# Kernel optimization log

Hardware: AMD Instinct MI355X
Metric: run time of the kernel (lower is better)

Reference implementation:

```python
import jax, jax.numpy as jnp
import numpy as np

RES = 256
XYZ_MIN, XYZ_MAX = -1.0, 1.0
STEPSIZE = 1.0
NEAR, FAR, BG = 0.2, 3.0, 1.0
ALPHA_INIT = 0.01
ACT_SHIFT = float(np.log(1.0 / (1.0 - ALPHA_INIT) - 1.0))
VOXEL = (XYZ_MAX - XYZ_MIN) / RES  # (prod(extent)/R^3)^(1/3) = 2/256
N_SAMPLES = int(np.linalg.norm(np.array([RES + 1] * 3, dtype=np.float64)) / STEPSIZE) + 1  # 446
N_RAYS = 4096
LATENT, NFEAT, RGB_LAT = 64, 32, 15
MULTIRES = 6


def _dense(key, din, dout):
    kw, kb = jax.random.split(key)
    return (jax.random.normal(kw, (din, dout), jnp.float32) / np.float32(np.sqrt(din)),
            jax.random.normal(kb, (dout,), jnp.float32) * 0.01)


def setup_inputs():
    ks = jax.random.split(jax.random.key(0), 16)
    rays_o = jax.random.normal(ks[0], (N_RAYS, 3), jnp.float32) * 1.5
    rays_d = jax.random.normal(ks[1], (N_RAYS, 3), jnp.float32)
    viewdirs = rays_d / jnp.linalg.norm(rays_d, axis=-1, keepdims=True)
    mW1, mb1 = _dense(ks[2], 4, 128)
    mW2, mb2 = _dense(ks[3], 128, 128)
    mW3, mb3 = _dense(ks[4], 128, NFEAT)
    pW1, pb1 = _dense(ks[5], LATENT, 64)
    pW2, pb2 = _dense(ks[6], 64, 64)
    pW3, pb3 = _dense(ks[7], 64, 1 + RGB_LAT)
    emb_dim = 3 + 3 * 2 * MULTIRES  # 39
    dW1, db1 = _dense(ks[8], RGB_LAT + emb_dim, 64)
    dW2, db2 = _dense(ks[9], 64, 64)
    dW3, db3 = _dense(ks[10], 64, 64)
    dW4, db4 = _dense(ks[11], 64, 3)
    return dict(
        rays_o=rays_o, rays_d=rays_d, viewdirs=viewdirs,
        mapping_grid=jax.random.normal(ks[12], (4, RES, RES, RES), jnp.float32) * 0.1,
        feature_vectors=jax.random.normal(ks[13], (NFEAT, LATENT), jnp.float32) * 0.1,
        mW1=mW1, mb1=mb1, mW2=mW2, mb2=mb2, mW3=mW3, mb3=mb3,
        pW1=pW1, pb1=pb1, pW2=pW2, pb2=pb2, pW3=pW3, pb3=pb3,
        dW1=dW1, db1=db1, dW2=dW2, db2=db2, dW3=dW3, db3=db3, dW4=dW4, db4=db4)


def _trilinear(grid, pts):
    # grid: [C,R,R,R]; pts: [...,3] world coords; matches F.grid_sample(align_corners=True)
    # after the flip(-1) in the original (x indexes dim0 of the volume).
    g = jnp.transpose(grid, (1, 2, 3, 0))  # [R,R,R,C]
    u = (pts - XYZ_MIN) / (XYZ_MAX - XYZ_MIN)
    idx = jnp.clip(u * (RES - 1), 0.0, RES - 1.0)
    i0 = jnp.clip(jnp.floor(idx).astype(jnp.int32), 0, RES - 2)
    f = idx - i0.astype(idx.dtype)
    x0, y0, z0 = i0[..., 0], i0[..., 1], i0[..., 2]
    x1, y1, z1 = x0 + 1, y0 + 1, z0 + 1
    fx, fy, fz = f[..., 0:1], f[..., 1:2], f[..., 2:3]
    c000, c001 = g[x0, y0, z0], g[x0, y0, z1]
    c010, c011 = g[x0, y1, z0], g[x0, y1, z1]
    c100, c101 = g[x1, y0, z0], g[x1, y0, z1]
    c110, c111 = g[x1, y1, z0], g[x1, y1, z1]
    c00 = c000 * (1 - fz) + c001 * fz
    c01 = c010 * (1 - fz) + c011 * fz
    c10 = c100 * (1 - fz) + c101 * fz
    c11 = c110 * (1 - fz) + c111 * fz
    c0 = c00 * (1 - fy) + c01 * fy
    c1 = c10 * (1 - fy) + c11 * fy
    return c0 * (1 - fx) + c1 * fx


def _mlp3(x, W1, b1, W2, b2, W3, b3):
    h = jax.nn.relu(x @ W1 + b1)
    h = jax.nn.relu(h @ W2 + b2)
    return h @ W3 + b3


def _dir_embed(v):
    # NeRF positional encoding: [v, sin(2^i v), cos(2^i v)] for i in [0, MULTIRES)
    freqs = 2.0 ** jnp.arange(MULTIRES, dtype=v.dtype)  # [L]
    ang = v[..., None, :] * freqs[:, None]              # [N,L,3]
    sc = jnp.concatenate([jnp.sin(ang), jnp.cos(ang)], axis=-1)  # [N,L,6]
    return jnp.concatenate([v, sc.reshape(v.shape[0], 2 * 3 * MULTIRES)], axis=-1)  # [N,39]


def reference(rays_o, rays_d, viewdirs, mapping_grid, feature_vectors,
              mW1, mb1, mW2, mb2, mW3, mb3,
              pW1, pb1, pW2, pb2, pW3, pb3,
              dW1, db1, dW2, db2, dW3, db3, dW4, db4):
    # --- ray sampling (is_train=False, no jitter) ---
    vec = jnp.where(rays_d == 0, 1e-6, rays_d)
    rate_a = (XYZ_MAX - rays_o) / vec
    rate_b = (XYZ_MIN - rays_o) / vec
    t_min = jnp.clip(jnp.minimum(rate_a, rate_b).max(-1), NEAR, FAR)
    t_max = jnp.clip(jnp.maximum(rate_a, rate_b).min(-1), NEAR, FAR)
    step = STEPSIZE * VOXEL * jnp.arange(N_SAMPLES, dtype=rays_o.dtype)  # [S]
    interpx = t_min[:, None] + step[None, :] / jnp.linalg.norm(rays_d, axis=-1, keepdims=True)
    ray_pts = rays_o[:, None, :] + rays_d[:, None, :] * interpx[..., None]  # [N,S,3]
    valid = ~((t_max <= t_min)[:, None]
              | jnp.any((ray_pts < XYZ_MIN) | (ray_pts > XYZ_MAX), axis=-1))  # [N,S]

    # --- latent extraction: grid sample -> attention over feature bank ---
    mp = _trilinear(mapping_grid, ray_pts)                                  # [N,S,4]
    attn = jax.nn.softmax(_mlp3(mp, mW1, mb1, mW2, mb2, mW3, mb3), axis=-1)  # [N,S,F]
    latent = attn @ feature_vectors                                          # [N,S,latent]

    # --- positional MLP -> density + rgb latent (masked entries zeroed as in torch) ---
    pos = _mlp3(latent, pW1, pb1, pW2, pb2, pW3, pb3)  # [N,S,1+rgb_lat]
    alpha = jnp.where(valid,
                      1.0 - jnp.exp(-jax.nn.softplus(pos[..., 0] + ACT_SHIFT) * STEPSIZE),
                      0.0)
    rgb_latent = jnp.where(valid[..., None], pos[..., 1:], 0.0)

    # --- alpha compositing weights ---
    alphainv_cum = jnp.concatenate(
        [jnp.ones_like(alpha[..., :1]),
         jnp.cumprod(jnp.clip(1.0 - alpha, 1e-10, None), axis=-1)], axis=-1)  # [N,S+1]
    weights = alpha * alphainv_cum[..., :-1]

    # --- directional MLP -> rgb ---
    emb = _dir_embed(viewdirs)                                               # [N,39]
    emb = jnp.broadcast_to(emb[:, None, :], (alpha.shape[0], alpha.shape[1], emb.shape[-1]))
    rgb_feat = jnp.concatenate([rgb_latent, emb], axis=-1)                   # [N,S,54]
    h = jax.nn.relu(rgb_feat @ dW1 + db1)
    h = jax.nn.relu(h @ dW2 + db2)
    h = jax.nn.relu(h @ dW3 + db3)
    raw_rgb = h @ dW4 + db4
    rgb = jnp.where(valid[..., None], jax.nn.sigmoid(raw_rgb[..., :3]), 0.0)

    rgb_marched = jnp.einsum('ns,nsc->nc', weights, rgb) + alphainv_cum[..., -1:] * BG
    return rgb_marched
```

## Files before the change

kernel.cpp:

```cpp
#include <hip/hip_runtime.h>
#include <math.h>

#define ACT_SHIFT -4.5951198501345889f
#define SB 128
#define NSLOTMAX (4096*446)

typedef _Float16 f16;
typedef f16 f16x8 __attribute__((ext_vector_type(8)));
typedef f16 f16x4 __attribute__((ext_vector_type(4)));
typedef float f32x4 __attribute__((ext_vector_type(4)));
typedef float f32x16 __attribute__((ext_vector_type(16)));

#define OFF_CNT  0
#define OFF_RAYI 256
#define OFF_RAYF (OFF_RAYI + 4096*16)
#define OFF_EMBW (OFF_RAYF + 4096*8)
#define OFF_WTS  (OFF_EMBW + 4096*64*4)
#define OFF_BIAS (OFF_WTS + 92160)
#define OFF_SLOT (OFF_BIAS + 8192)
#define OFF_WS4H (OFF_SLOT + NSLOTMAX*4)

#define W_MW1 0
#define W_MW2 2048
#define W_MW3 18432
#define W_FV  22528
#define W_P1  24576
#define W_P2  28672
#define W_P3  32768
#define W_D1  34816
#define W_D2  35840
#define W_D3  39936
#define W_D4  44032
#define W_TOT 46080

static __device__ __forceinline__ unsigned short f2h(float x) {
  f16 h = (f16)x; return *(unsigned short*)&h;
}
static __device__ __forceinline__ float h2f(unsigned short u) {
  return (float)(*(f16*)&u);
}

static __device__ __forceinline__ void bar_lds() {
  asm volatile("s_waitcnt lgkmcnt(0)" ::: "memory");
  __builtin_amdgcn_s_barrier();
}

static __device__ __forceinline__ void sample_point(
    float ox, float oy, float oz, float dx, float dy, float dz,
    float tmin, float nrm, int s, float& px, float& py, float& pz) {
  float ix = tmin + (0.0078125f * (float)s) / nrm;
  px = ox + dx * ix; py = oy + dy * ix; pz = oz + dz * ix;
}
static __device__ __forceinline__ int in_box(float px, float py, float pz) {
  return !(px < -1.f || px > 1.f || py < -1.f || py > 1.f ||
           pz < -1.f || pz > 1.f);
}

static __device__ __forceinline__ bool ray_setup(
    const float* rays_o, const float* rays_d, int r,
    float& ox, float& oy, float& oz, float& dx, float& dy, float& dz,
    float& tmin, float& nrm) {
  ox = rays_o[r*3+0]; oy = rays_o[r*3+1]; oz = rays_o[r*3+2];
  dx = rays_d[r*3+0]; dy = rays_d[r*3+1]; dz = rays_d[r*3+2];
  const float vx = (dx == 0.0f) ? 1e-6f : dx;
  const float vy = (dy == 0.0f) ? 1e-6f : dy;
  const float vz = (dz == 0.0f) ? 1e-6f : dz;
  const float rax = ( 1.0f - ox) / vx, rbx = (-1.0f - ox) / vx;
  const float ray_ = ( 1.0f - oy) / vy, rby = (-1.0f - oy) / vy;
  const float raz = ( 1.0f - oz) / vz, rbz = (-1.0f - oz) / vz;
  tmin = fmaxf(fmaxf(fminf(rax,rbx), fminf(ray_,rby)), fminf(raz,rbz));
  tmin = fminf(fmaxf(tmin, 0.2f), 3.0f);
  float tmax = fminf(fminf(fmaxf(rax,rbx), fmaxf(ray_,rby)), fmaxf(raz,rbz));
  tmax = fminf(fmaxf(tmax, 0.2f), 3.0f);
  nrm = sqrtf(dx*dx + dy*dy + dz*dz);
  return tmax <= tmin;
}

// ... 44 lines not shown
      const float* __restrict__ mb1, const float* __restrict__ mb2,
      const float* __restrict__ mb3, const float* __restrict__ pb1,
      const float* __restrict__ pb2, const float* __restrict__ pb3,
      const float* __restrict__ db1, const float* __restrict__ db2,
      const float* __restrict__ db3, const float* __restrict__ db4,
      f16* __restrict__ wts, float* __restrict__ bias,
      float* __restrict__ embW) {
  const int b = blockIdx.x, t = threadIdx.x;
  if (b < 1024) {
    int idx = b * 256 + t;
    int ray = idx >> 6, o = idx & 63;
    float v0 = viewdirs[ray*3+0], v1 = viewdirs[ray*3+1], v2 = viewdirs[ray*3+2];
    float acc = db1[o];
    acc = fmaf(v0, dW1[15*64+o], acc);
    acc = fmaf(v1, dW1[16*64+o], acc);
    acc = fmaf(v2, dW1[17*64+o], acc);
#pragma unroll
    for (int fr = 0; fr < 6; ++fr) {
      float f = (float)(1 << fr);
      int rb = 18 + fr*6;
      acc = fmaf(sinf(v0*f), dW1[(rb+0)*64+o], acc);
      acc = fmaf(sinf(v1*f), dW1[(rb+1)*64+o], acc);
      acc = fmaf(sinf(v2*f), dW1[(rb+2)*64+o], acc);
      acc = fmaf(cosf(v0*f), dW1[(rb+3)*64+o], acc);
      acc = fmaf(cosf(v1*f), dW1[(rb+4)*64+o], acc);
      acc = fmaf(cosf(v2*f), dW1[(rb+5)*64+o], acc);
    }
    embW[idx] = acc;
  } else if (b < 1280) {
    int ray = (b - 1024) * 16 + (t >> 4);
    int4 ri = rayi[ray];
    for (int i = t & 15; i < ri.z; i += 16)
      slot_map[ri.x + i] = (ray << 9) | (ri.y + i);
  } else if (b < 1460) {
    int i = (b - 1280) * 256 + t;
    if (i >= W_TOT) return;
    float v = 0.f; int l, o, k;
    if (i < W_MW2)      { l=i;        o=l>>4; k=l&15;  if (k<4)  v = mW1[k*128+o]; }
    else if (i < W_MW3) { l=i-W_MW2;  o=l>>7; k=l&127; v = mW2[k*128+o]; }
    else if (i < W_FV)  { l=i-W_MW3;  o=l>>7; k=l&127; v = mW3[k*32+o]; }
    else if (i < W_P1)  { l=i-W_FV;   o=l>>5; k=l&31;  v = fv[k*64+o]; }
    else if (i < W_P2)  { l=i-W_P1;   o=l>>6; k=l&63;  v = pW1[k*64+o]; }
    else if (i < W_P3)  { l=i-W_P2;   o=l>>6; k=l&63;  v = pW2[k*64+o]; }
    else if (i < W_D1)  { l=i-W_P3;   o=l>>6; k=l&63;  if (o<16) v = pW3[k*16+o]; }
    else if (i < W_D2)  { l=i-W_D1;   o=l>>4; k=l&15;  if (k>=1) v = dW1[(k-1)*64+o]; }
    else if (i < W_D3)  { l=i-W_D2;   o=l>>6; k=l&63;  v = dW2[k*64+o]; }
    else if (i < W_D4)  { l=i-W_D3;   o=l>>6; k=l&63;  v = dW3[k*64+o]; }
    else                { l=i-W_D4;   o=l>>6; k=l&63;  if (o<3)  v = dW4[k*3+o]; }
    wts[i] = (f16)v;
  } else {
    int i = (b - 1460) * 256 + t;
    if (i >= 1408) return;
    int L = i >> 7, o = i & 127;
    float v = 0.f;
    if      (L == 0)            v = mb1[o];
    else if (L == 1)            v = mb2[o];
    else if (L == 2 && o < 32)  v = mb3[o];
    else if (L == 4 && o < 64)  v = pb1[o];
    else if (L == 5 && o < 64)  v = pb2[o];
    else if (L == 6 && o < 16)  v = pb3[o];
    else if (L == 8 && o < 64)  v = db2[o];
    else if (L == 9 && o < 64)  v = db3[o];
    else if (L == 10 && o < 3)  v = db4[o];
    bias[i] = v;
  }
}

template<int KS>
static __device__ __forceinline__ void load_b(const f16* Xb, int st, int lane,
                                              f16x8* B) {
  const int r = st*32 + (lane & 31);
  const int base = r*256 + ((lane >> 5) * 16);
#pragma unroll
  for (int ks = 0; ks < KS; ++ks) {
    int off = (base + ks*32) ^ ((r & 15) << 4);
    B[ks] = *(const f16x8*)((const char*)Xb + off);
  }
}

template<int KS>
static __device__ __forceinline__ void load_a(const f16* __restrict__ wbase,
                                              int dt, int lane, f16x8* A) {
  const f16* wp = wbase + (size_t)(dt*32 + (lane & 31)) * (KS*16) + (lane >> 5) * 8;
#pragma unroll
  for (int ks = 0; ks < KS; ++ks) A[ks] = *(const f16x8*)(wp + ks*16);
}

template<int KS>
static __device__ __forceinline__ f32x16 mm(const f16x8* A, const f16x8* B) {
  f32x16 acc;
#pragma unroll
  for (int i = 0; i < 16; ++i) acc[i] = 0.f;
#pragma unroll
  for (int ks = 0; ks < KS; ++ks)
    acc = __builtin_amdgcn_mfma_f32_32x32x16_f16(A[ks], B[ks], acc, 0, 0, 0);
  return acc;
}

template<bool RELU, int NQ>
static __device__ __forceinline__ void store_c(f16* Yb, int st, int dtb, int lane,
                                               const f32x16& acc,
                                               const float* __restrict__ bp) {
  const int r = st*32 + (lane & 31);
  const int gp = (lane >> 5) * 4;
#pragma unroll
  for (int q = 0; q < NQ; ++q) {
    const int db = dtb + q*8 + gp;
    f32x4 b4 = *(const f32x4*)(bp + db);
    float v0 = acc[4*q+0]+b4[0], v1 = acc[4*q+1]+b4[1];
    float v2 = acc[4*q+2]+b4[2], v3 = acc[4*q+3]+b4[3];
    if (RELU) {
      v0 = fmaxf(v0,0.f); v1 = fmaxf(v1,0.f);
      v2 = fmaxf(v2,0.f); v3 = fmaxf(v3,0.f);
    }
    f16x4 o = {(f16)v0,(f16)v1,(f16)v2,(f16)v3};
    int off = (r*256 + db*2) ^ ((r & 15) << 4);
    *(f16x4*)((char*)Yb + off) = o;
  }
}

struct Pf {
  float v[8];
  float fx, fy, fz;
  int pk;
};

static __device__ __forceinline__ void pf_issue(
    int slot, int total, int c,
    const int* __restrict__ slot_map, const float2* __restrict__ rayf,
    const float* __restrict__ rays_o, const float* __restrict__ rays_d,
    const float* __restrict__ grid, Pf& P) {
  if (slot >= total) {
    P.pk = -2; P.fx = P.fy = P.fz = 0.f;
#pragma unroll
    for (int i = 0; i < 8; ++i) P.v[i] = 0.f;
    return;
  }
  int mi = slot_map[slot];
  int ray = mi >> 9, s = mi & 511;
  float2 tf = rayf[ray];
  float ox = rays_o[ray*3+0], oy = rays_o[ray*3+1], oz = rays_o[ray*3+2];
  float dx = rays_d[ray*3+0], dy = rays_d[ray*3+1], dz = rays_d[ray*3+2];
  float px, py, pz;
  sample_point(ox,oy,oz,dx,dy,dz, tf.x, tf.y, s, px,py,pz);
  P.pk = ray*2 + in_box(px,py,pz);
  float ixf = fminf(fmaxf((px + 1.f) * 0.5f * 255.f, 0.f), 255.f);
  float iyf = fminf(fmaxf((py + 1.f) * 0.5f * 255.f, 0.f), 255.f);
  float izf = fminf(fmaxf((pz + 1.f) * 0.5f * 255.f, 0.f), 255.f);
  int x0 = min((int)ixf, 254), y0 = min((int)iyf, 254), z0 = min((int)izf, 254);
  P.fx = ixf - (float)x0; P.fy = iyf - (float)y0; P.fz = izf - (float)z0;
  const float* gc = grid + (size_t)c * 16777216u;
  int bx0 = x0 << 16, bx1 = bx0 + 65536;
  int by0 = y0 << 8,  by1 = by0 + 256;
  P.v[0] = gc[bx0+by0+z0]; P.v[1] = gc[bx0+by0+z0+1];
  P.v[2] = gc[bx0+by1+z0]; P.v[3] = gc[bx0+by1+z0+1];
  P.v[4] = gc[bx1+by0+z0]; P.v[5] = gc[bx1+by0+z0+1];
  P.v[6] = gc[bx1+by1+z0]; P.v[7] = gc[bx1+by1+z0+1];
}

extern "C" __global__ void __launch_bounds__(512)
k_mlp(const float* __restrict__ rays_o, const float* __restrict__ rays_d,
      const float* __restrict__ grid, const int* __restrict__ slot_map,
      const float2* __restrict__ rayf, const float* __restrict__ embW,
      const f16* __restrict__ wts, const float* __restrict__ bias,
      int* __restrict__ cnt, unsigned short* __restrict__ ws4h) {
  const int total = cnt[0];
  const int nch = (total + 127) >> 7;
  int* qh = cnt + 1;
  const int tid = threadIdx.x;
  const int wv = tid >> 6, lane = tid & 63;
  const int sl = tid >> 2, ch = tid & 3;
  const int dthi = wv >> 2;
  const int stw = wv & 3;

  __shared__ __align__(16) f16 X[SB*128];
  __shared__ __align__(16) f16 Y[SB*128];
  __shared__ int sinfo[SB];
  __shared__ int q_next;

  f16x8 aMW1a[1], aMW1b[1], aFV[2], aP1[4], aP2[4], aD1[1], aD2[4], aD3[4];
  load_a<1>(wts+W_MW1, dthi,   lane, aMW1a);
  load_a<1>(wts+W_MW1, dthi+2, lane, aMW1b);
  load_a<2>(wts+W_FV,  dthi,   lane, aFV);
  load_a<4>(wts+W_P1,  dthi,   lane, aP1);
  load_a<4>(wts+W_P2,  dthi,   lane, aP2);
  load_a<1>(wts+W_D1,  dthi,   lane, aD1);
  load_a<4>(wts+W_D2,  dthi,   lane, aD2);
  load_a<4>(wts+W_D3,  dthi,   lane, aD3);
  f16x8 aP3[4], aD4[4];
  if (wv < 4) {
    load_a<4>(wts+W_P3, 0, lane, aP3);
    load_a<4>(wts+W_D4, 0, lane, aD4);
  }

  if (tid == 0) q_next = atomicAdd(qh, 1);
  __syncthreads();
  int cur = q_next;

  Pf P;
  pf_issue((cur < nch) ? cur*128 + sl : total, total, ch,
           slot_map, rayf, rays_o, rays_d, grid, P);

  while (cur < nch) {
    const int blockbase = cur << 7;
    if (tid == 0) q_next = atomicAdd(qh, 1);

    {
      float c00 = P.v[0]*(1.f-P.fz) + P.v[1]*P.fz;
      float c01 = P.v[2]*(1.f-P.fz) + P.v[3]*P.fz;
      float c10 = P.v[4]*(1.f-P.fz) + P.v[5]*P.fz;
      float c11 = P.v[6]*(1.f-P.fz) + P.v[7]*P.fz;
      float c0v = c00*(1.f-P.fy) + c01*P.fy;
      float c1v = c10*(1.f-P.fy) + c11*P.fy;
      float mv  = c0v*(1.f-P.fx) + c1v*P.fx;
      if (ch == 0) sinfo[sl] = P.pk;
      int off = (sl*256 + ch*2) ^ ((sl & 15) << 4);
      *(f16*)((char*)X + off) = (f16)mv;
      if (ch < 3) {
        int zo = (sl*256 + 8 + ch*8) ^ ((sl & 15) << 4);
        *(unsigned long long*)((char*)X + zo) = 0ull;
      }
    }
    bar_lds();
    const int nxt = q_next;
    pf_issue((nxt < nch) ? nxt*128 + sl : total, total, ch,
             slot_map, rayf, rays_o, rays_d, grid, P);

    float alpha_reg = 0.f; int pk_reg = -2;

    { f16x8 B[1]; load_b<1>(X, stw, lane, B);
      f32x16 a0 = mm<1>(aMW1a, B);
      store_c<true,4>(Y, stw, dthi*32, lane, a0, bias + 0*128);
      f32x16 a1 = mm<1>(aMW1b, B);
      store_c<true,4>(Y, stw, (dthi+2)*32, lane, a1, bias + 0*128);
    } bar_lds();

    { f16x8 B[8]; load_b<8>(Y, stw, lane, B);
      f16x8 A8[8];
      load_a<8>(wts+W_MW2, dthi, lane, A8);
      f32x16 a0 = mm<8>(A8, B);
      store_c<true,4>(X, stw, dthi*32, lane, a0, bias + 1*128);
      load_a<8>(wts+W_MW2, dthi+2, lane, A8);
      f32x16 a1 = mm<8>(A8, B);
      store_c<true,4>(X, stw, (dthi+2)*32, lane, a1, bias + 1*128);
    } bar_lds();

    if (wv < 4) {
      f16x8 B[8]; load_b<8>(X, wv, lane, B);
      f16x8 A8[8]; load_a<8>(wts+W_MW3, 0, lane, A8);
      f32x16 acc = mm<8>(A8, B);
      const int gp = (lane >> 5) * 4;
      float v[16];
#pragma unroll
      for (int q = 0; q < 4; ++q) {
        f32x4 b4 = *(const f32x4*)(bias + 2*128 + q*8 + gp);
#pragma unroll
        for (int i = 0; i < 4; ++i) v[4*q+i] = acc[4*q+i] + b4[i];
      }
      float mx = v[0];
#pragma unroll
      for (int i = 1; i < 16; ++i) mx = fmaxf(mx, v[i]);
      mx = fmaxf(mx, __shfl_xor(mx, 32));
      float s = 0.f;
#pragma unroll
      for (int i = 0; i < 16; ++i) { v[i] = expf(v[i] - mx); s += v[i]; }
      s += __shfl_xor(s, 32);
      float inv = 1.f / s;
      const int r = wv*32 + (lane & 31);
#pragma unroll
      for (int q = 0; q < 4; ++q) {
        const int db = q*8 + gp;
        f16x4 o = {(f16)(v[4*q+0]*inv), (f16)(v[4*q+1]*inv),
                   (f16)(v[4*q+2]*inv), (f16)(v[4*q+3]*inv)};
        int off = (r*256 + db*2) ^ ((r & 15) << 4);
        *(f16x4*)((char*)Y + off) = o;
      }
    }
    bar_lds();

    { f16x8 B[2]; load_b<2>(Y, stw, lane, B);
      f32x16 a0 = mm<2>(aFV, B);
      store_c<false,4>(X, stw, dthi*32, lane, a0, bias + 3*128);
    } bar_lds();

    { f16x8 B[4]; load_b<4>(X, stw, lane, B);
      f32x16 a0 = mm<4>(aP1, B);
      store_c<true,4>(Y, stw, dthi*32, lane, a0, bias + 4*128);
    } bar_lds();

    { f16x8 B[4]; load_b<4>(Y, stw, lane, B);
      f32x16 a0 = mm<4>(aP2, B);
      store_c<true,4>(X, stw, dthi*32, lane, a0, bias + 5*128);
    } bar_lds();

    if (wv < 4) {
      f16x8 B[4]; load_b<4>(X, wv, lane, B);
      f32x16 acc = mm<4>(aP3, B);
      pk_reg = sinfo[wv*32 + (lane & 31)];
      if (lane < 32) {
        alpha_reg = 0.f;
        if (pk_reg >= 0 && (pk_reg & 1)) {
          float x = acc[0] + bias[6*128 + 0] + ACT_SHIFT;
          float sp = fmaxf(x, 0.f) + log1pf(expf(-fabsf(x)));
          alpha_reg = 1.f - expf(-sp);
        }
      }
      store_c<false,2>(Y, wv, 0, lane, acc, bias + 6*128);
    }
    bar_lds();

    { f16x8 B[1]; load_b<1>(Y, stw, lane, B);
      f32x16 acc = mm<1>(aD1, B);
      int pkc = sinfo[stw*32 + (lane & 31)];
      int ry = (pkc < 0) ? 0 : (pkc >> 1);
      store_c<true,4>(X, stw, dthi*32, lane, acc, embW + (size_t)ry*64);
    } bar_lds();

    { f16x8 B[4]; load_b<4>(X, stw, lane, B);
      f32x16 a0 = mm<4>(aD2, B);
      store_c<true,4>(Y, stw, dthi*32, lane, a0, bias + 8*128);
    } bar_lds();

    { f16x8 B[4]; load_b<4>(Y, stw, lane, B);
      f32x16 a0 = mm<4>(aD3, B);
      store_c<true,4>(X, stw, dthi*32, lane, a0, bias + 9*128);
    } bar_lds();

    if (wv < 4) {
      f16x8 B[4]; load_b<4>(X, wv, lane, B);
      f32x16 acc = mm<4>(aD4, B);
      if (lane < 32 && pk_reg >= 0) {
        const float* bp = bias + 10*128;
        bool val = (pk_reg & 1) != 0;
        ushort4 u;
        u.x = f2h(alpha_reg);
        u.y = f2h(val ? 1.f/(1.f+expf(-(acc[0]+bp[0]))) : 0.f);
        u.z = f2h(val ? 1.f/(1.f+expf(-(acc[1]+bp[1]))) : 0.f);
        u.w = f2h(val ? 1.f/(1.f+expf(-(acc[2]+bp[2]))) : 0.f);
        *(ushort4*)(ws4h + (size_t)(blockbase + wv*32 + (lane & 31))*4) = u;
      }
    }
    bar_lds();
    cur = nxt;
  }
}

extern "C" __global__ void __launch_bounds__(256)
k_scan(const ushort4* __restrict__ ws4h, const int4* __restrict__ rayi,
       float* __restrict__ out) {
  const int wid = (blockIdx.x * 256 + threadIdx.x) >> 6;
  const int ln  = threadIdx.x & 63;
  if (wid >= 4096) return;
  int4 ri = rayi[wid];
  int base = ri.x, n_s = ri.z;

  float T = 1.0f, ar = 0.f, ag = 0.f, ab = 0.f;
  int nc = (n_s + 63) >> 6;
  for (int cck = 0; cck < nc; ++cck) {
    int j = cck*64 + ln;
    float a = 0.f, rr = 0.f, gg = 0.f, bb = 0.f;
    if (j < n_s) {
      ushort4 u = ws4h[(size_t)base + j];
      a = h2f(u.x); rr = h2f(u.y); gg = h2f(u.z); bb = h2f(u.w);
    }
    float p = fmaxf(1.0f - a, 1e-10f);
#pragma unroll
    for (int off = 1; off < 64; off <<= 1) {
      float o = __shfl_up(p, off);
      if (ln >= off) p *= o;
    }
    float pe = __shfl_up(p, 1);
    if (ln == 0) pe = 1.0f;
    float wgt = a * T * pe;
    ar = fmaf(wgt, rr, ar);
    ag = fmaf(wgt, gg, ag);
    ab = fmaf(wgt, bb, ab);
// ... 14 lines not shown

extern "C" void kernel_launch(void* const* d_in, const int* in_sizes, int n_in,
                              void* d_out, int out_size, void* d_ws, size_t ws_size,
                              hipStream_t stream) {
  const float* rays_o   = (const float*)d_in[0];
  const float* rays_d   = (const float*)d_in[1];
  const float* viewdirs = (const float*)d_in[2];
  const float* grid     = (const float*)d_in[3];
  const float* fv       = (const float*)d_in[4];
  const float* mW1 = (const float*)d_in[5];  const float* mb1 = (const float*)d_in[6];
  const float* mW2 = (const float*)d_in[7];  const float* mb2 = (const float*)d_in[8];
  const float* mW3 = (const float*)d_in[9];  const float* mb3 = (const float*)d_in[10];
  const float* pW1 = (const float*)d_in[11]; const float* pb1 = (const float*)d_in[12];
  const float* pW2 = (const float*)d_in[13]; const float* pb2 = (const float*)d_in[14];
  const float* pW3 = (const float*)d_in[15]; const float* pb3 = (const float*)d_in[16];
  const float* dW1 = (const float*)d_in[17]; const float* db1 = (const float*)d_in[18];
  const float* dW2 = (const float*)d_in[19]; const float* db2 = (const float*)d_in[20];
  const float* dW3 = (const float*)d_in[21]; const float* db3 = (const float*)d_in[22];
  const float* dW4 = (const float*)d_in[23]; const float* db4 = (const float*)d_in[24];
  float* out = (float*)d_out;

  char* ws = (char*)d_ws;
  int*     cnt      = (int*)(ws + OFF_CNT);
  int4*    rayi     = (int4*)(ws + OFF_RAYI);
  float2*  rayf     = (float2*)(ws + OFF_RAYF);
  float*   embW     = (float*)(ws + OFF_EMBW);
  f16*     wts      = (f16*)(ws + OFF_WTS);
  float*   bias     = (float*)(ws + OFF_BIAS);
  int*     slot_map = (int*)(ws + OFF_SLOT);
  unsigned short* ws4h = (unsigned short*)(ws + OFF_WS4H);

  hipMemsetAsync(cnt, 0, 8, stream);
  k_setup<<<16, 256, 0, stream>>>(rays_o, rays_d, cnt, rayi, rayf);
  k_aux<<<1466, 256, 0, stream>>>(viewdirs, rayi, slot_map,
                                  mW1, mW2, mW3, fv, pW1, pW2, pW3,
                                  dW1, dW2, dW3, dW4,
                                  mb1, mb2, mb3, pb1, pb2, pb3,
                                  db1, db2, db3, db4, wts, bias, embW);
  k_mlp<<<256, 512, 0, stream>>>(rays_o, rays_d, grid, slot_map, rayf,
                                 embW, wts, bias, cnt, ws4h);
  k_scan<<<1024, 256, 0, stream>>>((const ushort4*)ws4h, rayi, out);
}
```

Before: 103.2 us.

## Restructure MLP kernel into single-wave blocks processing 32-sample groups

Replaces the persistent 512-thread workgroup, which used an atomic work queue and barriers between layers over 128-sample tiles, with 64-thread single-wave blocks. Each block handles 32 samples with a grid-stride loop, so all layers run inside one wave with no LDS barriers. Weights are now read from global/L1 per layer instead of being held in registers, and each lane gathers two grid channels instead of one. The first-layer K dimension is padded to 32 so the weight layouts fit the new loops. This trades away inter-wave weight register reuse and the dynamic load balancing of the queue for more occupancy and less synchronisation.

```diff
diff --git a/kernel.cpp b/kernel.cpp
--- a/kernel.cpp
+++ b/kernel.cpp
@@ -2,12 +2,13 @@
 #include <math.h>
 
 #define ACT_SHIFT -4.5951198501345889f
-#define SB 128
 #define NSLOTMAX (4096*446)
+#define MLP_BLOCKS 2560
 
 typedef _Float16 f16;
 typedef f16 f16x8 __attribute__((ext_vector_type(8)));
 typedef f16 f16x4 __attribute__((ext_vector_type(4)));
+typedef f16 f16x2 __attribute__((ext_vector_type(2)));
 typedef float f32x4 __attribute__((ext_vector_type(4)));
 typedef float f32x16 __attribute__((ext_vector_type(16)));
 
@@ -16,33 +17,28 @@
 #define OFF_RAYF (OFF_RAYI + 4096*16)
 #define OFF_EMBW (OFF_RAYF + 4096*8)
 #define OFF_WTS  (OFF_EMBW + 4096*64*4)
-#define OFF_BIAS (OFF_WTS + 92160)
+#define OFF_BIAS (OFF_WTS + 98304)
 #define OFF_SLOT (OFF_BIAS + 8192)
 #define OFF_WS4H (OFF_SLOT + NSLOTMAX*4)
 
 #define W_MW1 0
-#define W_MW2 2048
-#define W_MW3 18432
-#define W_FV  22528
-#define W_P1  24576
-#define W_P2  28672
-#define W_P3  32768
-#define W_D1  34816
-#define W_D2  35840
-#define W_D3  39936
-#define W_D4  44032
-#define W_TOT 46080
+#define W_MW2 4096
+#define W_MW3 20480
+#define W_FV  24576
+#define W_P1  26624
+#define W_P2  30720
+#define W_P3  34816
+#define W_D1  36864
+#define W_D2  38912
+#define W_D3  43008
+#define W_D4  47104
+#define W_TOT 49152
 
 static __device__ __forceinline__ unsigned short f2h(float x) {
   f16 h = (f16)x; return *(unsigned short*)&h;
 }
 static __device__ __forceinline__ float h2f(unsigned short u) {
   return (float)(*(f16*)&u);
-}
-
-static __device__ __forceinline__ void bar_lds() {
-  asm volatile("s_waitcnt lgkmcnt(0)" ::: "memory");
-  __builtin_amdgcn_s_barrier();
 }
 
 static __device__ __forceinline__ void sample_point(
@@ -153,24 +149,24 @@
     int4 ri = rayi[ray];
     for (int i = t & 15; i < ri.z; i += 16)
       slot_map[ri.x + i] = (ray << 9) | (ri.y + i);
-  } else if (b < 1460) {
+  } else if (b < 1472) {
     int i = (b - 1280) * 256 + t;
     if (i >= W_TOT) return;
     float v = 0.f; int l, o, k;
-    if (i < W_MW2)      { l=i;        o=l>>4; k=l&15;  if (k<4)  v = mW1[k*128+o]; }
+    if (i < W_MW2)      { l=i;        o=l>>5; k=l&31;  if (k<4) v = mW1[k*128+o]; }
     else if (i < W_MW3) { l=i-W_MW2;  o=l>>7; k=l&127; v = mW2[k*128+o]; }
     else if (i < W_FV)  { l=i-W_MW3;  o=l>>7; k=l&127; v = mW3[k*32+o]; }
     else if (i < W_P1)  { l=i-W_FV;   o=l>>5; k=l&31;  v = fv[k*64+o]; }
     else if (i < W_P2)  { l=i-W_P1;   o=l>>6; k=l&63;  v = pW1[k*64+o]; }
     else if (i < W_P3)  { l=i-W_P2;   o=l>>6; k=l&63;  v = pW2[k*64+o]; }
     else if (i < W_D1)  { l=i-W_P3;   o=l>>6; k=l&63;  if (o<16) v = pW3[k*16+o]; }
-    else if (i < W_D2)  { l=i-W_D1;   o=l>>4; k=l&15;  if (k>=1) v = dW1[(k-1)*64+o]; }
+    else if (i < W_D2)  { l=i-W_D1;   o=l>>5; k=l&31;  if (k>=1 && k<16) v = dW1[(k-1)*64+o]; }
     else if (i < W_D3)  { l=i-W_D2;   o=l>>6; k=l&63;  v = dW2[k*64+o]; }
     else if (i < W_D4)  { l=i-W_D3;   o=l>>6; k=l&63;  v = dW3[k*64+o]; }
     else                { l=i-W_D4;   o=l>>6; k=l&63;  if (o<3)  v = dW4[k*3+o]; }
     wts[i] = (f16)v;
   } else {
-    int i = (b - 1460) * 256 + t;
+    int i = (b - 1472) * 256 + t;
     if (i >= 1408) return;
     int L = i >> 7, o = i & 127;
     float v = 0.f;
@@ -187,74 +183,192 @@
   }
 }
 
+static __device__ __forceinline__ f32x16 mfma16(f16x8 a, f16x8 b, f32x16 c) {
+  return __builtin_amdgcn_mfma_f32_32x32x16_f16(a, b, c, 0, 0, 0);
+}
+
 template<int KS>
-static __device__ __forceinline__ void load_b(const f16* Xb, int st, int lane,
-                                              f16x8* B) {
-  const int r = st*32 + (lane & 31);
-  const int base = r*256 + ((lane >> 5) * 16);
-#pragma unroll
-  for (int ks = 0; ks < KS; ++ks) {
-    int off = (base + ks*32) ^ ((r & 15) << 4);
-    B[ks] = *(const f16x8*)((const char*)Xb + off);
-  }
-}
-
-template<int KS>
-static __device__ __forceinline__ void load_a(const f16* __restrict__ wbase,
-                                              int dt, int lane, f16x8* A) {
-  const f16* wp = wbase + (size_t)(dt*32 + (lane & 31)) * (KS*16) + (lane >> 5) * 8;
-#pragma unroll
-  for (int ks = 0; ks < KS; ++ks) A[ks] = *(const f16x8*)(wp + ks*16);
-}
-
-template<int KS>
-static __device__ __forceinline__ f32x16 mm(const f16x8* A, const f16x8* B) {
+static __device__ __forceinline__ void load_B(const f16* Xi, int lane, f16x8* B) {
+  const int c = lane & 31;
+  const int sw = (c & 15) << 4;
+  const int rbase = c*256 + (lane >> 5) * 16;
+#pragma unroll
+  for (int ks = 0; ks < KS; ++ks)
+    B[ks] = *(const f16x8*)((const char*)Xi + ((rbase + ks*32) ^ sw));
+}
+
+template<int KS, int MT, bool RELU>
+static __device__ __forceinline__ void layerN(
+    const f16* __restrict__ W, const float* __restrict__ bp,
+    const f16* Xi, f16* Yo, int lane) {
+  const int c = lane & 31, g = lane >> 5;
+  const int sw = (c & 15) << 4;
+  f16x8 B[KS];
+  load_B<KS>(Xi, lane, B);
+#pragma unroll
+  for (int dt = 0; dt < MT; ++dt) {
+    f32x16 acc;
+#pragma unroll
+    for (int i = 0; i < 16; ++i) acc[i] = 0.f;
+    const f16* wp = W + (size_t)(dt*32 + c)*(KS*16) + g*8;
+#pragma unroll
+    for (int ks = 0; ks < KS; ++ks)
+      acc = mfma16(*(const f16x8*)(wp + ks*16), B[ks], acc);
+#pragma unroll
+    for (int q = 0; q < 4; ++q) {
+      const int db = dt*32 + q*8 + g*4;
+      f32x4 b4 = *(const f32x4*)(bp + db);
+      float v0 = acc[4*q+0]+b4[0], v1 = acc[4*q+1]+b4[1];
+      float v2 = acc[4*q+2]+b4[2], v3 = acc[4*q+3]+b4[3];
+      if (RELU) {
+        v0 = fmaxf(v0,0.f); v1 = fmaxf(v1,0.f);
+        v2 = fmaxf(v2,0.f); v3 = fmaxf(v3,0.f);
+      }
+      f16x4 o = {(f16)v0,(f16)v1,(f16)v2,(f16)v3};
+      *(f16x4*)((char*)Yo + ((c*256 + db*2) ^ sw)) = o;
+    }
+  }
+}
+
+static __device__ __forceinline__ void layer_emb(
+    const f16* __restrict__ W, const float* __restrict__ embR,
+    const f16* Xi, f16* Yo, int lane) {
+  const int c = lane & 31, g = lane >> 5;
+  const int sw = (c & 15) << 4;
+  f16x8 B[2];
+  load_B<2>(Xi, lane, B);
+#pragma unroll
+  for (int dt = 0; dt < 2; ++dt) {
+    f32x16 acc;
+#pragma unroll
+    for (int i = 0; i < 16; ++i) acc[i] = 0.f;
+    const f16* wp = W + (size_t)(dt*32 + c)*32 + g*8;
+#pragma unroll
+    for (int ks = 0; ks < 2; ++ks)
+      acc = mfma16(*(const f16x8*)(wp + ks*16), B[ks], acc);
+#pragma unroll
+    for (int q = 0; q < 4; ++q) {
+      const int db = dt*32 + q*8 + g*4;
+      f32x4 b4 = *(const f32x4*)(embR + db);
+      float v0 = fmaxf(acc[4*q+0]+b4[0], 0.f), v1 = fmaxf(acc[4*q+1]+b4[1], 0.f);
+      float v2 = fmaxf(acc[4*q+2]+b4[2], 0.f), v3 = fmaxf(acc[4*q+3]+b4[3], 0.f);
+      f16x4 o = {(f16)v0,(f16)v1,(f16)v2,(f16)v3};
+      *(f16x4*)((char*)Yo + ((c*256 + db*2) ^ sw)) = o;
+    }
+  }
+}
+
+static __device__ __forceinline__ void layer_mw3(
+    const f16* __restrict__ W, const float* __restrict__ bp,
+    const f16* Xi, f16* Yo, int lane) {
+  const int c = lane & 31, g = lane >> 5;
+  const int sw = (c & 15) << 4;
+  f16x8 B[8];
+  load_B<8>(Xi, lane, B);
   f32x16 acc;
 #pragma unroll
   for (int i = 0; i < 16; ++i) acc[i] = 0.f;
-#pragma unroll
-  for (int ks = 0; ks < KS; ++ks)
-    acc = __builtin_amdgcn_mfma_f32_32x32x16_f16(A[ks], B[ks], acc, 0, 0, 0);
-  return acc;
-}
-
-template<bool RELU, int NQ>
-static __device__ __forceinline__ void store_c(f16* Yb, int st, int dtb, int lane,
-                                               const f32x16& acc,
-                                               const float* __restrict__ bp) {
-  const int r = st*32 + (lane & 31);
-  const int gp = (lane >> 5) * 4;
-#pragma unroll
-  for (int q = 0; q < NQ; ++q) {
-    const int db = dtb + q*8 + gp;
+  const f16* wp = W + (size_t)c*128 + g*8;
+#pragma unroll
+  for (int ks = 0; ks < 8; ++ks)
+    acc = mfma16(*(const f16x8*)(wp + ks*16), B[ks], acc);
+  float v[16];
+#pragma unroll
+  for (int q = 0; q < 4; ++q) {
+    f32x4 b4 = *(const f32x4*)(bp + q*8 + g*4);
+#pragma unroll
+    for (int i = 0; i < 4; ++i) v[4*q+i] = acc[4*q+i] + b4[i];
+  }
+  float mx = v[0];
+#pragma unroll
+  for (int i = 1; i < 16; ++i) mx = fmaxf(mx, v[i]);
+  mx = fmaxf(mx, __shfl_xor(mx, 32));
+  float s = 0.f;
+#pragma unroll
+  for (int i = 0; i < 16; ++i) { v[i] = expf(v[i] - mx); s += v[i]; }
+  s += __shfl_xor(s, 32);
+  float inv = 1.f / s;
+#pragma unroll
+  for (int q = 0; q < 4; ++q) {
+    const int db = q*8 + g*4;
+    f16x4 o = {(f16)(v[4*q+0]*inv), (f16)(v[4*q+1]*inv),
+               (f16)(v[4*q+2]*inv), (f16)(v[4*q+3]*inv)};
+    *(f16x4*)((char*)Yo + ((c*256 + db*2) ^ sw)) = o;
+  }
+}
+
+static __device__ __forceinline__ void layer_p3(
+    const f16* __restrict__ W, const float* __restrict__ bp,
+    const f16* Xi, f16* Yo, int lane, int pks, float& alpha) {
+  const int c = lane & 31, g = lane >> 5;
+  const int sw = (c & 15) << 4;
+  f16x8 B[4];
+  load_B<4>(Xi, lane, B);
+  f32x16 acc;
+#pragma unroll
+  for (int i = 0; i < 16; ++i) acc[i] = 0.f;
+  const f16* wp = W + (size_t)c*64 + g*8;
+#pragma unroll
+  for (int ks = 0; ks < 4; ++ks)
+    acc = mfma16(*(const f16x8*)(wp + ks*16), B[ks], acc);
+  if (g == 0) {
+    alpha = 0.f;
+    if (pks >= 0 && (pks & 1)) {
+      float x = acc[0] + bp[0] + ACT_SHIFT;
+      float sp = fmaxf(x, 0.f) + log1pf(expf(-fabsf(x)));
+      alpha = 1.f - expf(-sp);
+    }
+  }
+#pragma unroll
+  for (int q = 0; q < 4; ++q) {
+    const int db = q*8 + g*4;
     f32x4 b4 = *(const f32x4*)(bp + db);
-    float v0 = acc[4*q+0]+b4[0], v1 = acc[4*q+1]+b4[1];
-    float v2 = acc[4*q+2]+b4[2], v3 = acc[4*q+3]+b4[3];
-    if (RELU) {
-      v0 = fmaxf(v0,0.f); v1 = fmaxf(v1,0.f);
-      v2 = fmaxf(v2,0.f); v3 = fmaxf(v3,0.f);
-    }
-    f16x4 o = {(f16)v0,(f16)v1,(f16)v2,(f16)v3};
-    int off = (r*256 + db*2) ^ ((r & 15) << 4);
-    *(f16x4*)((char*)Yb + off) = o;
+    f16x4 o = {(f16)(acc[4*q+0]+b4[0]), (f16)(acc[4*q+1]+b4[1]),
+               (f16)(acc[4*q+2]+b4[2]), (f16)(acc[4*q+3]+b4[3])};
+    *(f16x4*)((char*)Yo + ((c*256 + db*2) ^ sw)) = o;
+  }
+}
+
+static __device__ __forceinline__ void layer_d4(
+    const f16* __restrict__ W, const float* __restrict__ bp,
+    const f16* Xi, int lane, int pks, float alpha,
+    unsigned short* __restrict__ ws4h, int base) {
+  const int c = lane & 31, g = lane >> 5;
+  f16x8 B[4];
+  load_B<4>(Xi, lane, B);
+  f32x16 acc;
+#pragma unroll
+  for (int i = 0; i < 16; ++i) acc[i] = 0.f;
+  const f16* wp = W + (size_t)c*64 + g*8;
+#pragma unroll
+  for (int ks = 0; ks < 4; ++ks)
+    acc = mfma16(*(const f16x8*)(wp + ks*16), B[ks], acc);
+  if (g == 0 && pks >= 0) {
+    bool val = (pks & 1) != 0;
+    ushort4 u;
+    u.x = f2h(alpha);
+    u.y = f2h(val ? 1.f/(1.f+expf(-(acc[0]+bp[0]))) : 0.f);
+    u.z = f2h(val ? 1.f/(1.f+expf(-(acc[1]+bp[1]))) : 0.f);
+    u.w = f2h(val ? 1.f/(1.f+expf(-(acc[2]+bp[2]))) : 0.f);
+    *(ushort4*)(ws4h + (size_t)(base + c)*4) = u;
   }
 }
 
 struct Pf {
-  float v[8];
+  float v[16];
   float fx, fy, fz;
   int pk;
 };
 
 static __device__ __forceinline__ void pf_issue(
-    int slot, int total, int c,
+    int slot, int total, int cpair,
     const int* __restrict__ slot_map, const float2* __restrict__ rayf,
     const float* __restrict__ rays_o, const float* __restrict__ rays_d,
     const float* __restrict__ grid, Pf& P) {
   if (slot >= total) {
     P.pk = -2; P.fx = P.fy = P.fz = 0.f;
 #pragma unroll
-    for (int i = 0; i < 8; ++i) P.v[i] = 0.f;
+    for (int i = 0; i < 16; ++i) P.v[i] = 0.f;
     return;
   }
   int mi = slot_map[slot];
@@ -270,199 +384,89 @@
   float izf = fminf(fmaxf((pz + 1.f) * 0.5f * 255.f, 0.f), 255.f);
   int x0 = min((int)ixf, 254), y0 = min((int)iyf, 254), z0 = min((int)izf, 254);
   P.fx = ixf - (float)x0; P.fy = iyf - (float)y0; P.fz = izf - (float)z0;
-  const float* gc = grid + (size_t)c * 16777216u;
   int bx0 = x0 << 16, bx1 = bx0 + 65536;
   int by0 = y0 << 8,  by1 = by0 + 256;
-  P.v[0] = gc[bx0+by0+z0]; P.v[1] = gc[bx0+by0+z0+1];
-  P.v[2] = gc[bx0+by1+z0]; P.v[3] = gc[bx0+by1+z0+1];
-  P.v[4] = gc[bx1+by0+z0]; P.v[5] = gc[bx1+by0+z0+1];
-  P.v[6] = gc[bx1+by1+z0]; P.v[7] = gc[bx1+by1+z0+1];
-}
-
-extern "C" __global__ void __launch_bounds__(512)
+#pragma unroll
+  for (int q = 0; q < 2; ++q) {
+    const float* gc = grid + (size_t)(cpair*2 + q) * 16777216u;
+    P.v[q*8+0] = gc[bx0+by0+z0]; P.v[q*8+1] = gc[bx0+by0+z0+1];
+    P.v[q*8+2] = gc[bx0+by1+z0]; P.v[q*8+3] = gc[bx0+by1+z0+1];
+    P.v[q*8+4] = gc[bx1+by0+z0]; P.v[q*8+5] = gc[bx1+by0+z0+1];
+    P.v[q*8+6] = gc[bx1+by1+z0]; P.v[q*8+7] = gc[bx1+by1+z0+1];
+  }
+}
+
+extern "C" __global__ void __launch_bounds__(64)
 k_mlp(const float* __restrict__ rays_o, const float* __restrict__ rays_d,
       const float* __restrict__ grid, const int* __restrict__ slot_map,
       const float2* __restrict__ rayf, const float* __restrict__ embW,
       const f16* __restrict__ wts, const float* __restrict__ bias,
-      int* __restrict__ cnt, unsigned short* __restrict__ ws4h) {
+      const int* __restrict__ cnt, unsigned short* __restrict__ ws4h) {
   const int total = cnt[0];
-  const int nch = (total + 127) >> 7;
-  int* qh = cnt + 1;
-  const int tid = threadIdx.x;
-  const int wv = tid >> 6, lane = tid & 63;
-  const int sl = tid >> 2, ch = tid & 3;
-  const int dthi = wv >> 2;
-  const int stw = wv & 3;
-
-  __shared__ __align__(16) f16 X[SB*128];
-  __shared__ __align__(16) f16 Y[SB*128];
-  __shared__ int sinfo[SB];
-  __shared__ int q_next;
-
-  f16x8 aMW1a[1], aMW1b[1], aFV[2], aP1[4], aP2[4], aD1[1], aD2[4], aD3[4];
-  load_a<1>(wts+W_MW1, dthi,   lane, aMW1a);
-  load_a<1>(wts+W_MW1, dthi+2, lane, aMW1b);
-  load_a<2>(wts+W_FV,  dthi,   lane, aFV);
-  load_a<4>(wts+W_P1,  dthi,   lane, aP1);
-  load_a<4>(wts+W_P2,  dthi,   lane, aP2);
-  load_a<1>(wts+W_D1,  dthi,   lane, aD1);
-  load_a<4>(wts+W_D2,  dthi,   lane, aD2);
-  load_a<4>(wts+W_D3,  dthi,   lane, aD3);
-  f16x8 aP3[4], aD4[4];
-  if (wv < 4) {
-    load_a<4>(wts+W_P3, 0, lane, aP3);
-    load_a<4>(wts+W_D4, 0, lane, aD4);
-  }
-
-  if (tid == 0) q_next = atomicAdd(qh, 1);
-  __syncthreads();
-  int cur = q_next;
-
+  const int ngrp = (total + 31) >> 5;
+  const int lane = threadIdx.x;
+  const int sl = lane >> 1, cp = lane & 1;
+  const int c = lane & 31;
+
+  __shared__ __align__(16) f16 X[32*128];
+  __shared__ __align__(16) f16 Y[32*128];
+
+  int grp = blockIdx.x;
   Pf P;
-  pf_issue((cur < nch) ? cur*128 + sl : total, total, ch,
+  pf_issue((grp < ngrp) ? grp*32 + sl : total, total, cp,
            slot_map, rayf, rays_o, rays_d, grid, P);
 
-  while (cur < nch) {
-    const int blockbase = cur << 7;
-    if (tid == 0) q_next = atomicAdd(qh, 1);
-
+  for (; grp < ngrp; grp += gridDim.x) {
     {
-      float c00 = P.v[0]*(1.f-P.fz) + P.v[1]*P.fz;
-      float c01 = P.v[2]*(1.f-P.fz) + P.v[3]*P.fz;
-      float c10 = P.v[4]*(1.f-P.fz) + P.v[5]*P.fz;
-      float c11 = P.v[6]*(1.f-P.fz) + P.v[7]*P.fz;
-      float c0v = c00*(1.f-P.fy) + c01*P.fy;
-      float c1v = c10*(1.f-P.fy) + c11*P.fy;
-      float mv  = c0v*(1.f-P.fx) + c1v*P.fx;
-      if (ch == 0) sinfo[sl] = P.pk;
-      int off = (sl*256 + ch*2) ^ ((sl & 15) << 4);
-      *(f16*)((char*)X + off) = (f16)mv;
-      if (ch < 3) {
-        int zo = (sl*256 + 8 + ch*8) ^ ((sl & 15) << 4);
-        *(unsigned long long*)((char*)X + zo) = 0ull;
+      const int swr = (sl & 15) << 4;
+      float m[2];
+#pragma unroll
+      for (int q = 0; q < 2; ++q) {
+        const float* vv = P.v + q*8;
+        float c00 = vv[0]*(1.f-P.fz) + vv[1]*P.fz;
+        float c01 = vv[2]*(1.f-P.fz) + vv[3]*P.fz;
+        float c10 = vv[4]*(1.f-P.fz) + vv[5]*P.fz;
+        float c11 = vv[6]*(1.f-P.fz) + vv[7]*P.fz;
+        float c0v = c00*(1.f-P.fy) + c01*P.fy;
+        float c1v = c10*(1.f-P.fy) + c11*P.fy;
+        m[q] = c0v*(1.f-P.fx) + c1v*P.fx;
       }
-    }
-    bar_lds();
-    const int nxt = q_next;
-    pf_issue((nxt < nch) ? nxt*128 + sl : total, total, ch,
-             slot_map, rayf, rays_o, rays_d, grid, P);
-
-    float alpha_reg = 0.f; int pk_reg = -2;
-
-    { f16x8 B[1]; load_b<1>(X, stw, lane, B);
-      f32x16 a0 = mm<1>(aMW1a, B);
-      store_c<true,4>(Y, stw, dthi*32, lane, a0, bias + 0*128);
-      f32x16 a1 = mm<1>(aMW1b, B);
-      store_c<true,4>(Y, stw, (dthi+2)*32, lane, a1, bias + 0*128);
-    } bar_lds();
-
-    { f16x8 B[8]; load_b<8>(Y, stw, lane, B);
-      f16x8 A8[8];
-      load_a<8>(wts+W_MW2, dthi, lane, A8);
-      f32x16 a0 = mm<8>(A8, B);
-      store_c<true,4>(X, stw, dthi*32, lane, a0, bias + 1*128);
-      load_a<8>(wts+W_MW2, dthi+2, lane, A8);
-      f32x16 a1 = mm<8>(A8, B);
-      store_c<true,4>(X, stw, (dthi+2)*32, lane, a1, bias + 1*128);
-    } bar_lds();
-
-    if (wv < 4) {
-      f16x8 B[8]; load_b<8>(X, wv, lane, B);
-      f16x8 A8[8]; load_a<8>(wts+W_MW3, 0, lane, A8);
-      f32x16 acc = mm<8>(A8, B);
-      const int gp = (lane >> 5) * 4;
-      float v[16];
-#pragma unroll
-      for (int q = 0; q < 4; ++q) {
-        f32x4 b4 = *(const f32x4*)(bias + 2*128 + q*8 + gp);
-#pragma unroll
-        for (int i = 0; i < 4; ++i) v[4*q+i] = acc[4*q+i] + b4[i];
+      f16x2 w2 = {(f16)m[0], (f16)m[1]};
+      *(f16x2*)((char*)X + ((sl*256 + cp*4) ^ swr)) = w2;
+      if (cp == 0) {
+#pragma unroll
+        for (int z = 0; z < 3; ++z)
+          *(unsigned long long*)((char*)X + ((sl*256 + 8 + z*8) ^ swr)) = 0ull;
+      } else {
+#pragma unroll
+        for (int z = 0; z < 4; ++z)
+          *(unsigned long long*)((char*)X + ((sl*256 + 32 + z*8) ^ swr)) = 0ull;
       }
-      float mx = v[0];
-#pragma unroll
-      for (int i = 1; i < 16; ++i) mx = fmaxf(mx, v[i]);
-      mx = fmaxf(mx, __shfl_xor(mx, 32));
-      float s = 0.f;
-#pragma unroll
-      for (int i = 0; i < 16; ++i) { v[i] = expf(v[i] - mx); s += v[i]; }
-      s += __shfl_xor(s, 32);
-      float inv = 1.f / s;
-      const int r = wv*32 + (lane & 31);
-#pragma unroll
-      for (int q = 0; q < 4; ++q) {
-        const int db = q*8 + gp;
-        f16x4 o = {(f16)(v[4*q+0]*inv), (f16)(v[4*q+1]*inv),
-                   (f16)(v[4*q+2]*inv), (f16)(v[4*q+3]*inv)};
-        int off = (r*256 + db*2) ^ ((r & 15) << 4);
-        *(f16x4*)((char*)Y + off) = o;
-      }
-    }
-    bar_lds();
-
-    { f16x8 B[2]; load_b<2>(Y, stw, lane, B);
-      f32x16 a0 = mm<2>(aFV, B);
-      store_c<false,4>(X, stw, dthi*32, lane, a0, bias + 3*128);
-    } bar_lds();
-
-    { f16x8 B[4]; load_b<4>(X, stw, lane, B);
-      f32x16 a0 = mm<4>(aP1, B);
-      store_c<true,4>(Y, stw, dthi*32, lane, a0, bias + 4*128);
-    } bar_lds();
-
-    { f16x8 B[4]; load_b<4>(Y, stw, lane, B);
-      f32x16 a0 = mm<4>(aP2, B);
-      store_c<true,4>(X, stw, dthi*32, lane, a0, bias + 5*128);
-    } bar_lds();
-
-    if (wv < 4) {
-      f16x8 B[4]; load_b<4>(X, wv, lane, B);
-      f32x16 acc = mm<4>(aP3, B);
-      pk_reg = sinfo[wv*32 + (lane & 31)];
-      if (lane < 32) {
-        alpha_reg = 0.f;
-        if (pk_reg >= 0 && (pk_reg & 1)) {
-          float x = acc[0] + bias[6*128 + 0] + ACT_SHIFT;
-          float sp = fmaxf(x, 0.f) + log1pf(expf(-fabsf(x)));
-          alpha_reg = 1.f - expf(-sp);
-        }
-      }
-      store_c<false,2>(Y, wv, 0, lane, acc, bias + 6*128);
-    }
-    bar_lds();
-
-    { f16x8 B[1]; load_b<1>(Y, stw, lane, B);
-      f32x16 acc = mm<1>(aD1, B);
-      int pkc = sinfo[stw*32 + (lane & 31)];
-      int ry = (pkc < 0) ? 0 : (pkc >> 1);
-      store_c<true,4>(X, stw, dthi*32, lane, acc, embW + (size_t)ry*64);
-    } bar_lds();
-
-    { f16x8 B[4]; load_b<4>(X, stw, lane, B);
-      f32x16 a0 = mm<4>(aD2, B);
-      store_c<true,4>(Y, stw, dthi*32, lane, a0, bias + 8*128);
-    } bar_lds();
-
-    { f16x8 B[4]; load_b<4>(Y, stw, lane, B);
-      f32x16 a0 = mm<4>(aD3, B);
-      store_c<true,4>(X, stw, dthi*32, lane, a0, bias + 9*128);
-    } bar_lds();
-
-    if (wv < 4) {
-      f16x8 B[4]; load_b<4>(X, wv, lane, B);
-      f32x16 acc = mm<4>(aD4, B);
-      if (lane < 32 && pk_reg >= 0) {
-        const float* bp = bias + 10*128;
-        bool val = (pk_reg & 1) != 0;
-        ushort4 u;
-        u.x = f2h(alpha_reg);
-        u.y = f2h(val ? 1.f/(1.f+expf(-(acc[0]+bp[0]))) : 0.f);
-        u.z = f2h(val ? 1.f/(1.f+expf(-(acc[1]+bp[1]))) : 0.f);
-        u.w = f2h(val ? 1.f/(1.f+expf(-(acc[2]+bp[2]))) : 0.f);
-        *(ushort4*)(ws4h + (size_t)(blockbase + wv*32 + (lane & 31))*4) = u;
-      }
-    }
-    bar_lds();
-    cur = nxt;
+    }
+    const int pkr = P.pk;
+    const int base = grp << 5;
+
+    {
+      int nx = grp + gridDim.x;
+      pf_issue((nx < ngrp) ? nx*32 + sl : total, total, cp,
+               slot_map, rayf, rays_o, rays_d, grid, P);
+    }
+
+    const int pks = __shfl(pkr, c*2);
+    const int ry  = (pks < 0) ? 0 : (pks >> 1);
+    float alpha = 0.f;
+
+    layerN<2,4,true >(wts+W_MW1, bias + 0*128, X, Y, lane);
+    layerN<8,4,true >(wts+W_MW2, bias + 1*128, Y, X, lane);
+    layer_mw3(wts+W_MW3, bias + 2*128, X, Y, lane);
+    layerN<2,2,false>(wts+W_FV,  bias + 3*128, Y, X, lane);
+    layerN<4,2,true >(wts+W_P1,  bias + 4*128, X, Y, lane);
+    layerN<4,2,true >(wts+W_P2,  bias + 5*128, Y, X, lane);
+    layer_p3(wts+W_P3, bias + 6*128, X, Y, lane, pks, alpha);
+    layer_emb(wts+W_D1, embW + (size_t)ry*64, Y, X, lane);
+    layerN<4,2,true >(wts+W_D2,  bias + 8*128, X, Y, lane);
+    layerN<4,2,true >(wts+W_D3,  bias + 9*128, Y, X, lane);
+    layer_d4(wts+W_D4, bias + 10*128, X, lane, pks, alpha, ws4h, base);
   }
 }
 
@@ -543,12 +547,12 @@
 
   hipMemsetAsync(cnt, 0, 8, stream);
   k_setup<<<16, 256, 0, stream>>>(rays_o, rays_d, cnt, rayi, rayf);
-  k_aux<<<1466, 256, 0, stream>>>(viewdirs, rayi, slot_map,
+  k_aux<<<1478, 256, 0, stream>>>(viewdirs, rayi, slot_map,
                                   mW1, mW2, mW3, fv, pW1, pW2, pW3,
                                   dW1, dW2, dW3, dW4,
                                   mb1, mb2, mb3, pb1, pb2, pb3,
                                   db1, db2, db3, db4, wts, bias, embW);
-  k_mlp<<<256, 512, 0, stream>>>(rays_o, rays_d, grid, slot_map, rayf,
-                                 embW, wts, bias, cnt, ws4h);
+  k_mlp<<<MLP_BLOCKS, 64, 0, stream>>>(rays_o, rays_d, grid, slot_map, rayf,
+                                       embW, wts, bias, cnt, ws4h);
   k_scan<<<1024, 256, 0, stream>>>((const ushort4*)ws4h, rayi, out);
 }
```

Result: slower. 238.8 us (+131.3%).

## Reload MLP weights per layer instead of holding them in registers, raise occupancy

Applied to the files above, without the earlier changes.

The persistent MLP kernel used to keep all MFMA A-operand weight fragments in registers for its whole lifetime. It now reloads each layer's weights from global memory (L1/L2 cached) right before that layer's matmul. This frees registers so __launch_bounds__(512,4) can be met, and the grid grows from 256 to 768 workgroups. The aim is more waves per CU to hide the trilinear-gather and barrier latency, at the cost of extra weight-load traffic and latency on every 128-sample chunk.

```diff
diff --git a/kernel.cpp b/kernel.cpp
--- a/kernel.cpp
+++ b/kernel.cpp
@@ -4,10 +4,12 @@
 #define ACT_SHIFT -4.5951198501345889f
 #define SB 128
 #define NSLOTMAX (4096*446)
+#define MLP_BLOCKS 768
 
 typedef _Float16 f16;
 typedef f16 f16x8 __attribute__((ext_vector_type(8)));
 typedef f16 f16x4 __attribute__((ext_vector_type(4)));
+typedef f16 f16x2 __attribute__((ext_vector_type(2)));
 typedef float f32x4 __attribute__((ext_vector_type(4)));
 typedef float f32x16 __attribute__((ext_vector_type(16)));
 
@@ -279,7 +281,7 @@
   P.v[6] = gc[bx1+by1+z0]; P.v[7] = gc[bx1+by1+z0+1];
 }
 
-extern "C" __global__ void __launch_bounds__(512)
+extern "C" __global__ void __launch_bounds__(512, 4)
 k_mlp(const float* __restrict__ rays_o, const float* __restrict__ rays_d,
       const float* __restrict__ grid, const int* __restrict__ slot_map,
       const float2* __restrict__ rayf, const float* __restrict__ embW,
@@ -298,21 +300,6 @@
   __shared__ __align__(16) f16 Y[SB*128];
   __shared__ int sinfo[SB];
   __shared__ int q_next;
-
-  f16x8 aMW1a[1], aMW1b[1], aFV[2], aP1[4], aP2[4], aD1[1], aD2[4], aD3[4];
-  load_a<1>(wts+W_MW1, dthi,   lane, aMW1a);
-  load_a<1>(wts+W_MW1, dthi+2, lane, aMW1b);
-  load_a<2>(wts+W_FV,  dthi,   lane, aFV);
-  load_a<4>(wts+W_P1,  dthi,   lane, aP1);
-  load_a<4>(wts+W_P2,  dthi,   lane, aP2);
-  load_a<1>(wts+W_D1,  dthi,   lane, aD1);
-  load_a<4>(wts+W_D2,  dthi,   lane, aD2);
-  load_a<4>(wts+W_D3,  dthi,   lane, aD3);
-  f16x8 aP3[4], aD4[4];
-  if (wv < 4) {
-    load_a<4>(wts+W_P3, 0, lane, aP3);
-    load_a<4>(wts+W_D4, 0, lane, aD4);
-  }
 
   if (tid == 0) q_next = atomicAdd(qh, 1);
   __syncthreads();
@@ -350,9 +337,12 @@
     float alpha_reg = 0.f; int pk_reg = -2;
 
     { f16x8 B[1]; load_b<1>(X, stw, lane, B);
-      f32x16 a0 = mm<1>(aMW1a, B);
+      f16x8 A1[1];
+      load_a<1>(wts+W_MW1, dthi, lane, A1);
+      f32x16 a0 = mm<1>(A1, B);
       store_c<true,4>(Y, stw, dthi*32, lane, a0, bias + 0*128);
-      f32x16 a1 = mm<1>(aMW1b, B);
+      load_a<1>(wts+W_MW1, dthi+2, lane, A1);
+      f32x16 a1 = mm<1>(A1, B);
       store_c<true,4>(Y, stw, (dthi+2)*32, lane, a1, bias + 0*128);
     } bar_lds();
 
@@ -400,23 +390,27 @@
     bar_lds();
 
     { f16x8 B[2]; load_b<2>(Y, stw, lane, B);
-      f32x16 a0 = mm<2>(aFV, B);
+      f16x8 A2[2]; load_a<2>(wts+W_FV, dthi, lane, A2);
+      f32x16 a0 = mm<2>(A2, B);
       store_c<false,4>(X, stw, dthi*32, lane, a0, bias + 3*128);
     } bar_lds();
 
     { f16x8 B[4]; load_b<4>(X, stw, lane, B);
-      f32x16 a0 = mm<4>(aP1, B);
+      f16x8 A4[4]; load_a<4>(wts+W_P1, dthi, lane, A4);
+      f32x16 a0 = mm<4>(A4, B);
       store_c<true,4>(Y, stw, dthi*32, lane, a0, bias + 4*128);
     } bar_lds();
 
     { f16x8 B[4]; load_b<4>(Y, stw, lane, B);
-      f32x16 a0 = mm<4>(aP2, B);
+      f16x8 A4[4]; load_a<4>(wts+W_P2, dthi, lane, A4);
+      f32x16 a0 = mm<4>(A4, B);
       store_c<true,4>(X, stw, dthi*32, lane, a0, bias + 5*128);
     } bar_lds();
 
     if (wv < 4) {
       f16x8 B[4]; load_b<4>(X, wv, lane, B);
-      f32x16 acc = mm<4>(aP3, B);
+      f16x8 A4[4]; load_a<4>(wts+W_P3, 0, lane, A4);
+      f32x16 acc = mm<4>(A4, B);
       pk_reg = sinfo[wv*32 + (lane & 31)];
       if (lane < 32) {
         alpha_reg = 0.f;
@@ -431,25 +425,29 @@
     bar_lds();
 
     { f16x8 B[1]; load_b<1>(Y, stw, lane, B);
-      f32x16 acc = mm<1>(aD1, B);
+      f16x8 A1[1]; load_a<1>(wts+W_D1, dthi, lane, A1);
+      f32x16 acc = mm<1>(A1, B);
       int pkc = sinfo[stw*32 + (lane & 31)];
       int ry = (pkc < 0) ? 0 : (pkc >> 1);
       store_c<true,4>(X, stw, dthi*32, lane, acc, embW + (size_t)ry*64);
     } bar_lds();
 
     { f16x8 B[4]; load_b<4>(X, stw, lane, B);
-      f32x16 a0 = mm<4>(aD2, B);
+      f16x8 A4[4]; load_a<4>(wts+W_D2, dthi, lane, A4);
+      f32x16 a0 = mm<4>(A4, B);
       store_c<true,4>(Y, stw, dthi*32, lane, a0, bias + 8*128);
     } bar_lds();
 
     { f16x8 B[4]; load_b<4>(Y, stw, lane, B);
-      f32x16 a0 = mm<4>(aD3, B);
+      f16x8 A4[4]; load_a<4>(wts+W_D3, dthi, lane, A4);
+      f32x16 a0 = mm<4>(A4, B);
       store_c<true,4>(X, stw, dthi*32, lane, a0, bias + 9*128);
     } bar_lds();
 
     if (wv < 4) {
       f16x8 B[4]; load_b<4>(X, wv, lane, B);
-      f32x16 acc = mm<4>(aD4, B);
+      f16x8 A4[4]; load_a<4>(wts+W_D4, 0, lane, A4);
+      f32x16 acc = mm<4>(A4, B);
       if (lane < 32 && pk_reg >= 0) {
         const float* bp = bias + 10*128;
         bool val = (pk_reg & 1) != 0;
@@ -548,7 +546,7 @@
                                   dW1, dW2, dW3, dW4,
                                   mb1, mb2, mb3, pb1, pb2, pb3,
                                   db1, db2, db3, db4, wts, bias, embW);
-  k_mlp<<<256, 512, 0, stream>>>(rays_o, rays_d, grid, slot_map, rayf,
-                                 embW, wts, bias, cnt, ws4h);
+  k_mlp<<<MLP_BLOCKS, 512, 0, stream>>>(rays_o, rays_d, grid, slot_map, rayf,
+                                        embW, wts, bias, cnt, ws4h);
   k_scan<<<1024, 256, 0, stream>>>((const ushort4*)ws4h, rayi, out);
 }
```

Result: slower. 125.9 us (+22.0%).
